# Optimization experiments

Hardware: AMD Instinct MI355X
Metric: run time of the kernel (lower is better)

The kernel has to match this reference:

```python
import jax, jax.numpy as jnp
import numpy as np

MU = 255          # mu-law levels - 1
H = 64            # block_hidden_size
SKIP = 256        # skip_size
NL = 24           # num_layers
CYC = 6           # cycle_size -> dilation = 2**(i % CYC)
UPK = 4           # upsample conv kernel/stride
REP = 75          # upsample repeat
LF = 80           # local_features_size
B = 2
LLEN = 64                      # local (spectrogram) frames
SLEN = LLEN * UPK * REP        # 19200 signal samples


def setup_inputs() -> dict:
    key = jax.random.key(0)
    ks = jax.random.split(key, 16)
    s = 0.1
    rn = lambda k, shape: jax.random.normal(k, shape, jnp.float32) * s
    return {
        "local_features": jax.random.normal(ks[0], (B, LLEN, LF), jnp.float32),
        "gold_signal": jax.random.randint(ks[1], (B, SLEN), 0, MU + 1, jnp.int32),
        "embed_W": rn(ks[2], (H, MU + 1)),          # 1x1 conv (mu+1 -> H), as matrix
        "embed_b": rn(ks[3], (H,)),
        "up_W": rn(ks[4], (LF, LF, UPK)),           # ConvTranspose1d weight [in, out, k]
        "up_b": rn(ks[5], (LF,)),
        "cond_W": rn(ks[6], (NL * 2 * H, LF)),      # 1x1 conv LF -> NL*2H
        "cond_b": rn(ks[7], (NL * 2 * H,)),
        "dil_W": rn(ks[8], (NL, 2 * H, H, 2)),      # dilated causal conv, kernel 2
        "dil_b": rn(ks[9], (NL, 2 * H)),
        "skip_W": rn(ks[10], (NL, SKIP, H)),
        "skip_b": rn(ks[11], (NL, SKIP)),
        "res_W": rn(ks[12], (NL - 1, H, H)),        # no residual conv on last layer
        "res_b": rn(ks[13], (NL - 1, H)),
        "out_W1": rn(ks[14], (MU + 1, SKIP)),       # out conv 1 (no bias)
        "out_W2": rn(ks[15], (MU + 1, MU + 1)),     # out conv 2 (no bias)
    }


def reference(local_features, gold_signal, embed_W, embed_b, up_W, up_b,
              cond_W, cond_b, dil_W, dil_b, skip_W, skip_b, res_W, res_b,
              out_W1, out_W2):
    Bv = local_features.shape[0]
    # --- conditional features upsample ---
    x = jnp.transpose(local_features, (0, 2, 1))                     # [B, LF, Lloc]
    # ConvTranspose1d with kernel == stride == UPK: each frame emits UPK frames
    up = jnp.einsum('bct,cok->botk', x, up_W).reshape(Bv, LF, -1)    # [B, LF, Lloc*UPK]
    up = up + up_b[None, :, None]
    up = jnp.repeat(up, REP, axis=-1)                                # [B, LF, SLEN]
    cond = jnp.einsum('oc,bct->bot', cond_W, up) + cond_b[None, :, None]
    L = cond.shape[-1]
    cond = cond.reshape(Bv, NL, 2 * H, L)                            # per-layer 2H channels
    # --- embed mu-law one-hot signal (one-hot matmul == gather) ---
    sig = jnp.transpose(embed_W[:, gold_signal], (1, 0, 2)) + embed_b[None, :, None]  # [B, H, L]
    # --- residual blocks ---
    skip_sum = jnp.zeros((Bv, SKIP, L), cond.dtype)
    for i in range(NL):
        d = 2 ** (i % CYC)
        prev = jnp.pad(sig, ((0, 0), (0, 0), (d, 0)))[:, :, :L]      # causal shift by dilation
        a = (jnp.einsum('oc,bct->bot', dil_W[i, :, :, 0], prev)
             + jnp.einsum('oc,bct->bot', dil_W[i, :, :, 1], sig)
             + dil_b[i][None, :, None] + cond[:, i])
        z = jnp.tanh(a[:, :H]) * jax.nn.sigmoid(a[:, H:])            # gated activation
        skip_sum = skip_sum + jnp.einsum('oc,bct->bot', skip_W[i], z) + skip_b[i][None, :, None]
        if i < NL - 1:
            sig = sig + jnp.einsum('oc,bct->bot', res_W[i], z) + res_b[i][None, :, None]
    # --- output head: ReLU -> 1x1 -> ReLU -> 1x1 -> log_softmax over levels ---
    h = jax.nn.relu(skip_sum)
    h = jax.nn.relu(jnp.einsum('oc,bct->bot', out_W1, h))
    logits = jnp.einsum('oc,bct->bot', out_W2, h)
    return jax.nn.log_softmax(logits, axis=1)                        # [B, mu+1, SLEN]
```

## Files before the change

kernel.cpp:

```cpp
#include <hip/hip_runtime.h>
#include <math.h>

#define MU1   256
#define H     64
#define H2    128
#define SKIPC 256
#define NL    24
#define LF    80
#define UPK   4
#define REP   75
#define BB    2
#define LLEN  64
#define LL    19200

using bf16x8 = __attribute__((ext_vector_type(8))) short;
using bf16x4 = __attribute__((ext_vector_type(4))) short;
using f32x4  = __attribute__((ext_vector_type(4))) float;

__device__ __forceinline__ float b2f(short s) {
    union { unsigned u; float f; } v; v.u = ((unsigned)(unsigned short)s) << 16; return v.f;
}
__device__ __forceinline__ short f2b(float f) {
    union { float f; unsigned u; } v; v.f = f;
    unsigned r = (v.u + 0x7fff + ((v.u >> 16) & 1)) >> 16;
    return (short)r;
}

__global__ __launch_bounds__(256) void prep_kernel(
    const float* __restrict__ dil_W,  const float* __restrict__ skip_W,
    const float* __restrict__ res_W,  const float* __restrict__ embed_W,
    const float* __restrict__ embed_b,const float* __restrict__ cond_W,
    const float* __restrict__ out_W1, const float* __restrict__ out_W2,
    const float* __restrict__ skip_b,
    short* __restrict__ dil_Wb, short* __restrict__ sWt,
    short* __restrict__ res_Wb, short* __restrict__ embed_allb,
    float* __restrict__ cond_Wt, short* __restrict__ W1b,
    short* __restrict__ W2b, float* __restrict__ sbsum)
{
    int idx = blockIdx.x * 256 + threadIdx.x;
    const int n1 = NL * 2 * H2 * H;
    const int n2 = 12 * 256 * 128;
    const int n3 = (NL - 1) * H * H;
    const int n4 = MU1 * H;
    const int n5 = LF * NL * H2;
    const int n6 = MU1 * SKIPC;
    const int n7 = MU1 * MU1;
    if (idx < n1) {
        int c = idx & 63; int o = (idx >> 6) & 127;
        int k = (idx >> 13) & 1; int i = idx >> 14;
        dil_Wb[idx] = f2b(dil_W[((i * H2 + o) * H + c) * 2 + k]);
        return;
    }
    idx -= n1;
    if (idx < n2) {
        int kc = idx & 127; int s = (idx >> 7) & 255; int ck = idx >> 15;
        sWt[idx] = f2b(skip_W[((2 * ck + (kc >> 6)) * SKIPC + s) * H + (kc & 63)]);
        return;
    }
    idx -= n2;
    if (idx < n3) { res_Wb[idx] = f2b(res_W[idx]); return; }
    idx -= n3;
    if (idx < n4) {
        int h = idx & 63; int g = idx >> 6;
        embed_allb[idx] = f2b(embed_W[h * MU1 + g] + embed_b[h]);
        return;
    }
    idx -= n4;
    if (idx < n5) {
        int o = idx % (NL * H2); int c = idx / (NL * H2);
        cond_Wt[idx] = cond_W[o * LF + c];
        return;
    }
    idx -= n5;
    if (idx < n6) { W1b[idx] = f2b(out_W1[idx]); return; }
    idx -= n6;
    if (idx < n7) { W2b[idx] = f2b(out_W2[idx]); return; }
    idx -= n7;
    if (idx < SKIPC) {
        float a = 0.f;
        for (int i = 0; i < NL; i++) a += skip_b[i * SKIPC + idx];
        sbsum[idx] = a;
        return;
    }
}

__global__ __launch_bounds__(256) void embed_kernel(
    const int* __restrict__ gold, const short* __restrict__ eW,
    short* __restrict__ sig)
{
    int idx = blockIdx.x * 256 + threadIdx.x;
    if (idx >= BB * LL * 8) return;
    int ch = idx & 7; int bt = idx >> 3;
    int g = gold[bt];
    *(bf16x8*)(sig + (size_t)bt * H + ch * 8) = *(const bf16x8*)(eW + g * H + ch * 8);
}

__global__ __launch_bounds__(256) void cond_kernel(
    const float* __restrict__ lf, const float* __restrict__ up_W,
    const float* __restrict__ up_b, const float* __restrict__ cond_Wt,
    const float* __restrict__ cond_b, const float* __restrict__ dil_b,
    float* __restrict__ condS)
{
    __shared__ float s_up[LF];
    int j = blockIdx.x;
    int ot = blockIdx.y;
    int b = blockIdx.z;
    int frame = j >> 2, k = j & 3;
    int tid = threadIdx.x;
    if (tid < LF) {
        float a = up_b[tid];
        const float* lfr = lf + (b * LLEN + frame) * LF;
        #pragma unroll 8
        for (int c = 0; c < LF; ++c) a += lfr[c] * up_W[(c * LF + tid) * UPK + k];
        s_up[tid] = a;
    }
    __syncthreads();
    int o = ot * 256 + tid;
    float a = cond_b[o] + dil_b[o];
    #pragma unroll 8
    for (int c = 0; c < LF; ++c) a += cond_Wt[c * 3072 + o] * s_up[c];
    condS[((size_t)(b * 256 + j)) * 3072 + o] = a;
}

template<int DA, int DB, bool LASTPAIR>
__global__ __launch_bounds__(256) void pair_mfma(
    const short* __restrict__ sig_in, short* __restrict__ sig_out,
    short* __restrict__ z12,
    const short* __restrict__ dil_Wb_all,
    const short* __restrict__ res_Wb_all,
    const float* __restrict__ res_b_all,
    const float* __restrict__ condS,
    int p, int slot)
{
    __shared__ __align__(16) short sa[144][72];
    __shared__ __align__(16) short sb[128][72];
    __shared__ __align__(16) short sz[128][72];
    __shared__ float scond[2][3][128];

    const int iA = 2 * p, iB = 2 * p + 1;
    const int b = blockIdx.y;
    const int t0 = blockIdx.x * 96;
    const int tid = threadIdx.x;
    const int w = tid >> 6;
    const int lane = tid & 63;
    const int lr = lane & 15, lg = lane >> 4;
    const int c0 = (t0 >= 32) ? (t0 - 32) / 75 : 0;

    {
        const short* basein = sig_in + (size_t)b * LL * H;
        #pragma unroll
        for (int it = 0; it < 5; ++it) {
            int task = tid + it * 256;
            if (task < 1152) {
                int r = task >> 3, ch = task & 7;
                int t = t0 - 48 + r;
                bf16x8 v = {};
                if (t >= 0) v = *(const bf16x8*)(basein + (size_t)t * H + ch * 8);
                *(bf16x8*)&sa[r][ch * 8] = v;
            }
        }
        #pragma unroll
        for (int it = 0; it < 3; ++it) {
            int task = tid + it * 256;
            int sel = task >= 384;
            int cj = (task - sel * 384) >> 7;
            int o = task & 127;
            int col = c0 + cj; col = col > 255 ? 255 : col;
            scond[sel][cj][o] = condS[((size_t)(b * 256 + col)) * 3072 + (iA + sel) * 128 + o];
        }
    }
    __syncthreads();

    {
        const short* dW = dil_Wb_all + (size_t)iA * 2 * H2 * H;
        f32x4 acc[2][8];
        #pragma unroll
        for (int m = 0; m < 2; ++m)
            #pragma unroll
            for (int n = 0; n < 8; ++n) acc[m][n] = (f32x4){0.f, 0.f, 0.f, 0.f};
        bf16x8 afA[2][4];
        #pragma unroll
        for (int m = 0; m < 2; ++m) {
            int rc = 16 + 16 * (2 * w + m) + lr;
            afA[m][0] = *(const bf16x8*)&sa[rc - DA][lg * 8];
            afA[m][1] = *(const bf16x8*)&sa[rc - DA][32 + lg * 8];
            afA[m][2] = *(const bf16x8*)&sa[rc][lg * 8];
            afA[m][3] = *(const bf16x8*)&sa[rc][32 + lg * 8];
        }
        #pragma unroll
        for (int n = 0; n < 8; ++n)
            #pragma unroll
            for (int kk = 0; kk < 4; ++kk) {
                bf16x8 bw = *(const bf16x8*)(dW + (((kk >> 1) * H2 + 16 * n + lr) * H) + (kk & 1) * 32 + lg * 8);
                acc[0][n] = __builtin_amdgcn_mfma_f32_16x16x32_bf16(afA[0][kk], bw, acc[0][n], 0, 0, 0);
                acc[1][n] = __builtin_amdgcn_mfma_f32_16x16x32_bf16(afA[1][kk], bw, acc[1][n], 0, 0, 0);
            }
        #pragma unroll
        for (int m = 0; m < 2; ++m)
            #pragma unroll
            for (int n = 0; n < 4; ++n)
                #pragma unroll
                for (int r = 0; r < 4; ++r) {
                    int relt = -32 + 16 * (2 * w + m) + 4 * lg + r;
                    int t = t0 + relt;
                    int o = 16 * n + lr;
                    short zb = 0;
                    if (t >= 0) {
                        int ci = t / 75 - c0;
                        float av = acc[m][n][r] + scond[0][ci][o];
                        float gv = acc[m][n + 4][r] + scond[0][ci][64 + o];
                        float th = 1.f - 2.f / (__expf(2.f * av) + 1.f);
                        float sg = 1.f / (1.f + __expf(-gv));
                        zb = f2b(th * sg);
                    }
                    sz[relt + 32][o] = zb;
                }
    }
    __syncthreads();

    #pragma unroll
    for (int it = 0; it < 3; ++it) {
        int task = tid + it * 256;
        int r = task >> 3, ch = task & 7;
        *(bf16x8*)(z12 + ((size_t)((slot * BB + b) * LL) + t0 + r) * 128 + ch * 8)
            = *(const bf16x8*)&sz[32 + r][ch * 8];
    }

    {
        const short* rW = res_Wb_all + (size_t)iA * H * H;
        const float* rb_ = res_b_all + (size_t)iA * H;
        f32x4 rac[2][4];
        #pragma unroll
        for (int m = 0; m < 2; ++m)
            #pragma unroll
            for (int n = 0; n < 4; ++n) rac[m][n] = (f32x4){0.f, 0.f, 0.f, 0.f};
        bf16x8 za[2][2];
        #pragma unroll
        for (int m = 0; m < 2; ++m) {
            int row = 16 * (2 * w + m) + lr;
            za[m][0] = *(const bf16x8*)&sz[row][lg * 8];
            za[m][1] = *(const bf16x8*)&sz[row][32 + lg * 8];
        }
        #pragma unroll
        for (int n = 0; n < 4; ++n)
            #pragma unroll
            for (int kk = 0; kk < 2; ++kk) {
                bf16x8 bw = *(const bf16x8*)(rW + (16 * n + lr) * H + kk * 32 + lg * 8);
                rac[0][n] = __builtin_amdgcn_mfma_f32_16x16x32_bf16(za[0][kk], bw, rac[0][n], 0, 0, 0);
                rac[1][n] = __builtin_amdgcn_mfma_f32_16x16x32_bf16(za[1][kk], bw, rac[1][n], 0, 0, 0);
            }
        #pragma unroll
        for (int n = 0; n < 4; ++n) {
            float rbv = rb_[16 * n + lr];
            #pragma unroll
            for (int m = 0; m < 2; ++m)
                #pragma unroll
                for (int r = 0; r < 4; ++r) {
                    int relt = -32 + 16 * (2 * w + m) + 4 * lg + r;
                    int t = t0 + relt;
                    int c = 16 * n + lr;
                    short vb = 0;
                    if (t >= 0) vb = f2b(b2f(sa[relt + 48][c]) + rac[m][n][r] + rbv);
                    sb[relt + 32][c] = vb;
                }
        }
    }
    __syncthreads();

    {
        const short* dW = dil_Wb_all + (size_t)iB * 2 * H2 * H;
        f32x4 accF[6], accG[6];
        #pragma unroll
        for (int m = 0; m < 6; ++m) { accF[m] = (f32x4){0.f,0.f,0.f,0.f}; accG[m] = (f32x4){0.f,0.f,0.f,0.f}; }
        bf16x8 bwF[4], bwG[4];
        #pragma unroll
        for (int kk = 0; kk < 4; ++kk) {
            int oF = 16 * w + lr;
            bwF[kk] = *(const bf16x8*)(dW + (((kk >> 1) * H2 + oF) * H) + (kk & 1) * 32 + lg * 8);
            bwG[kk] = *(const bf16x8*)(dW + (((kk >> 1) * H2 + 64 + oF) * H) + (kk & 1) * 32 + lg * 8);
        }
        #pragma unroll
        for (int m = 0; m < 6; ++m) {
            int rc = 32 + 16 * m + lr;
            bf16x8 af[4];
            af[0] = *(const bf16x8*)&sb[rc - DB][lg * 8];
            af[1] = *(const bf16x8*)&sb[rc - DB][32 + lg * 8];
            af[2] = *(const bf16x8*)&sb[rc][lg * 8];
            af[3] = *(const bf16x8*)&sb[rc][32 + lg * 8];
            #pragma unroll
            for (int kk = 0; kk < 4; ++kk)
                accF[m] = __builtin_amdgcn_mfma_f32_16x16x32_bf16(af[kk], bwF[kk], accF[m], 0, 0, 0);
            #pragma unroll
            for (int kk = 0; kk < 4; ++kk)
                accG[m] = __builtin_amdgcn_mfma_f32_16x16x32_bf16(af[kk], bwG[kk], accG[m], 0, 0, 0);
        }
        #pragma unroll
        for (int m = 0; m < 6; ++m)
            #pragma unroll
            for (int r = 0; r < 4; ++r) {
                int relt = 16 * m + 4 * lg + r;
                int t = t0 + relt;
                int o = 16 * w + lr;
                int ci = t / 75 - c0;
                float av = accF[m][r] + scond[1][ci][o];
                float gv = accG[m][r] + scond[1][ci][64 + o];
                float th = 1.f - 2.f / (__expf(2.f * av) + 1.f);
                float sg = 1.f / (1.f + __expf(-gv));
                sz[relt][o] = f2b(th * sg);
            }
    }
    __syncthreads();

    #pragma unroll
    for (int it = 0; it < 3; ++it) {
        int task = tid + it * 256;
        int r = task >> 3, ch = task & 7;
        *(bf16x8*)(z12 + ((size_t)((slot * BB + b) * LL) + t0 + r) * 128 + 64 + ch * 8)
            = *(const bf16x8*)&sz[r][ch * 8];
    }

    if (!LASTPAIR) {
        const short* rW = res_Wb_all + (size_t)iB * H * H;
        const float* rb_ = res_b_all + (size_t)iB * H;
        int c = 16 * w + lr;
        f32x4 rac[6];
        #pragma unroll
        for (int m = 0; m < 6; ++m) rac[m] = (f32x4){0.f, 0.f, 0.f, 0.f};
        bf16x8 bwR[2];
        bwR[0] = *(const bf16x8*)(rW + c * H + lg * 8);
        bwR[1] = *(const bf16x8*)(rW + c * H + 32 + lg * 8);
        #pragma unroll
        for (int m = 0; m < 6; ++m) {
            bf16x8 z0 = *(const bf16x8*)&sz[16 * m + lr][lg * 8];
            bf16x8 z1 = *(const bf16x8*)&sz[16 * m + lr][32 + lg * 8];
            rac[m] = __builtin_amdgcn_mfma_f32_16x16x32_bf16(z0, bwR[0], rac[m], 0, 0, 0);
            rac[m] = __builtin_amdgcn_mfma_f32_16x16x32_bf16(z1, bwR[1], rac[m], 0, 0, 0);
        }
        float rbv = rb_[c];
        #pragma unroll
        for (int m = 0; m < 6; ++m)
            #pragma unroll
            for (int r = 0; r < 4; ++r) {
                int relt = 16 * m + 4 * lg + r;
                sa[relt][c] = f2b(b2f(sb[relt + 32][c]) + rac[m][r] + rbv);
            }
        __syncthreads();
        #pragma unroll
        for (int it = 0; it < 3; ++it) {
            int task = tid + it * 256;
            int r = task >> 3, ch = task & 7;
            *(bf16x8*)(sig_out + ((size_t)(b * LL + t0 + r)) * H + ch * 8)
                = *(const bf16x8*)&sa[r][ch * 8];
        }
    }
}

__global__ __launch_bounds__(256) void skip12_kernel(
    const short* __restrict__ z12, const short* __restrict__ sWt,
    short* __restrict__ skipP)
{
    __shared__ __align__(16) short s_a[2][64][136];
    const int b = blockIdx.y;
    const int t0 = blockIdx.x * 64;
    const int tid = threadIdx.x;
    const int w = tid >> 6;
    const int lane = tid & 63;
    const int lr = lane & 15, lg = lane >> 4;

    f32x4 acc[4][4];
    #pragma unroll
    for (int mt = 0; mt < 4; ++mt)
        #pragma unroll
        for (int nt = 0; nt < 4; ++nt) acc[mt][nt] = (f32x4){0.f, 0.f, 0.f, 0.f};

    #pragma unroll
    for (int it = 0; it < 4; ++it) {
        int task = tid + it * 256;
        int r = task >> 4, ch = task & 15;
        *(bf16x8*)&s_a[0][r][ch * 8] =
            *(const bf16x8*)(z12 + ((size_t)(b * LL) + t0 + r) * 128 + ch * 8);
    }
    __syncthreads();

    for (int ck = 0; ck < 6; ++ck) {
        if (ck < 5) {
            #pragma unroll
            for (int it = 0; it < 4; ++it) {
                int task = tid + it * 256;
                int r = task >> 4, ch = task & 15;
                *(bf16x8*)&s_a[(ck + 1) & 1][r][ch * 8] =
                    *(const bf16x8*)(z12 + ((size_t)(((ck + 1) * BB + b) * LL) + t0 + r) * 128 + ch * 8);
            }
        }
        const short* wbase = sWt + ((size_t)ck << 15);
        const short (*buf)[136] = s_a[ck & 1];
        #pragma unroll
        for (int kk = 0; kk < 4; ++kk) {
            bf16x8 afr[4];
            #pragma unroll
            for (int mt = 0; mt < 4; ++mt)
                afr[mt] = *(const bf16x8*)&buf[16 * mt + lr][32 * kk + 8 * lg];
            #pragma unroll
            for (int nt = 0; nt < 4; ++nt) {
                bf16x8 bw = *(const bf16x8*)(wbase + ((64 * w + 16 * nt + lr) << 7) + 32 * kk + 8 * lg);
                #pragma unroll
                for (int mt = 0; mt < 4; ++mt)
                    acc[mt][nt] = __builtin_amdgcn_mfma_f32_16x16x32_bf16(afr[mt], bw, acc[mt][nt], 0, 0, 0);
            }
        }
        __syncthreads();
    }

    #pragma unroll
    for (int mt = 0; mt < 4; ++mt)
        #pragma unroll
        for (int nt = 0; nt < 4; ++nt) {
            int s = 64 * w + 16 * nt + lr;
            #pragma unroll
            for (int reg = 0; reg < 4; ++reg) {
                int t = t0 + 16 * mt + 4 * lg + reg;
                skipP[((size_t)(b * LL) + t) * 256 + s] = f2b(acc[mt][nt][reg]);
            }
        }
}

__global__ __launch_bounds__(256) void skiphead_kernel(
    const short* __restrict__ z12, const short* __restrict__ sWt,
    const short* __restrict__ skipP, const float* __restrict__ sbsum,
    const short* __restrict__ W1b, const short* __restrict__ W2b,
    float* __restrict__ out)
{
    __shared__ __align__(16) unsigned char smem[36864];
    short (*s_ab)[64][136] = (short(*)[64][136])smem;
    short (*s_x)[264] = (short(*)[264])smem;
    float (*s_o)[68]  = (float(*)[68])smem;
    __shared__ float s_red[4][64];
    __shared__ float s_sb[256];

    const int b = blockIdx.y;
    const int t0 = blockIdx.x * 64;
    const int tid = threadIdx.x;
    const int w = tid >> 6;
    const int lane = tid & 63;
    const int lr = lane & 15, lg = lane >> 4;

    s_sb[tid] = sbsum[tid];

    f32x4 acc[4][4];
    #pragma unroll
    for (int mt = 0; mt < 4; ++mt)
        #pragma unroll
        for (int nt = 0; nt < 4; ++nt) acc[mt][nt] = (f32x4){0.f, 0.f, 0.f, 0.f};

    #pragma unroll
    for (int it = 0; it < 4; ++it) {
        int task = tid + it * 256;
        int r = task >> 4, ch = task & 15;
        *(bf16x8*)&s_ab[0][r][ch * 8] =
            *(const bf16x8*)(z12 + ((size_t)(b * LL) + t0 + r) * 128 + ch * 8);
    }
    __syncthreads();
    for (int ck = 0; ck < 6; ++ck) {
        if (ck < 5) {
            #pragma unroll
            for (int it = 0; it < 4; ++it) {
                int task = tid + it * 256;
                int r = task >> 4, ch = task & 15;
                *(bf16x8*)&s_ab[(ck + 1) & 1][r][ch * 8] =
                    *(const bf16x8*)(z12 + ((size_t)(((ck + 1) * BB + b) * LL) + t0 + r) * 128 + ch * 8);
            }
        }
        const short* wbase = sWt + ((size_t)(6 + ck) << 15);
        const short (*buf)[136] = s_ab[ck & 1];
        #pragma unroll
        for (int kk = 0; kk < 4; ++kk) {
            bf16x8 afr[4];
            #pragma unroll
            for (int mt = 0; mt < 4; ++mt)
                afr[mt] = *(const bf16x8*)&buf[16 * mt + lr][32 * kk + 8 * lg];
            #pragma unroll
            for (int nt = 0; nt < 4; ++nt) {
                bf16x8 bw = *(const bf16x8*)(wbase + ((64 * w + 16 * nt + lr) << 7) + 32 * kk + 8 * lg);
                #pragma unroll
                for (int mt = 0; mt < 4; ++mt)
                    acc[mt][nt] = __builtin_amdgcn_mfma_f32_16x16x32_bf16(afr[mt], bw, acc[mt][nt], 0, 0, 0);
            }
        }
        __syncthreads();
    }

    #pragma unroll
    for (int it = 0; it < 8; ++it) {
        int task = tid + it * 256;
        int r = task >> 5, ch = task & 31;
        *(bf16x8*)&s_x[r][ch * 8] =
            *(const bf16x8*)(skipP + ((size_t)(b * LL) + t0 + r) * 256 + ch * 8);
    }
    __syncthreads();
    #pragma unroll
    for (int mt = 0; mt < 4; ++mt)
        #pragma unroll
        for (int nt = 0; nt < 4; ++nt) {
            int s = 64 * w + 16 * nt + lr;
            #pragma unroll
            for (int reg = 0; reg < 4; ++reg) {
                int tl = 16 * mt + 4 * lg + reg;
                float v = acc[mt][nt][reg] + b2f(s_x[tl][s]) + s_sb[s];
                s_x[tl][s] = f2b(fmaxf(v, 0.f));
            }
        }
    __syncthreads();

    f32x4 acc1[4][4];
    #pragma unroll
    for (int mt = 0; mt < 4; ++mt)
        #pragma unroll
        for (int nt = 0; nt < 4; ++nt) acc1[mt][nt] = (f32x4){0.f, 0.f, 0.f, 0.f};
    #pragma unroll
    for (int kk = 0; kk < 8; ++kk) {
        bf16x8 afr[4];
        #pragma unroll
        for (int mt = 0; mt < 4; ++mt)
            afr[mt] = *(const bf16x8*)&s_x[16 * mt + lr][32 * kk + 8 * lg];
        #pragma unroll
        for (int nt = 0; nt < 4; ++nt) {
            bf16x8 bw = *(const bf16x8*)(W1b + ((size_t)(64 * w + 16 * nt + lr)) * MU1 + 32 * kk + 8 * lg);
            #pragma unroll
            for (int mt = 0; mt < 4; ++mt)
                acc1[mt][nt] = __builtin_amdgcn_mfma_f32_16x16x32_bf16(afr[mt], bw, acc1[mt][nt], 0, 0, 0);
        }
    }
    __syncthreads();
    #pragma unroll
    for (int mt = 0; mt < 4; ++mt)
        #pragma unroll
        for (int nt = 0; nt < 4; ++nt)
            #pragma unroll
            for (int reg = 0; reg < 4; ++reg) {
                int tl = 16 * mt + 4 * lg + reg;
                int o = 64 * w + 16 * nt + lr;
                s_x[tl][o] = f2b(fmaxf(acc1[mt][nt][reg], 0.f));
            }
    __syncthreads();

    f32x4 acc2[4][4];
    #pragma unroll
    for (int mt = 0; mt < 4; ++mt)
        #pragma unroll
        for (int nt = 0; nt < 4; ++nt) acc2[mt][nt] = (f32x4){0.f, 0.f, 0.f, 0.f};
    #pragma unroll
    for (int kk = 0; kk < 8; ++kk) {
        bf16x8 afr[4];
        #pragma unroll
        for (int mt = 0; mt < 4; ++mt)
            afr[mt] = *(const bf16x8*)&s_x[16 * mt + lr][32 * kk + 8 * lg];
        #pragma unroll
        for (int nt = 0; nt < 4; ++nt) {
            bf16x8 bw = *(const bf16x8*)(W2b + ((size_t)(64 * w + 16 * nt + lr)) * MU1 + 32 * kk + 8 * lg);
            #pragma unroll
            for (int mt = 0; mt < 4; ++mt)
                acc2[mt][nt] = __builtin_amdgcn_mfma_f32_16x16x32_bf16(afr[mt], bw, acc2[mt][nt], 0, 0, 0);
        }
    }

    float mv[4][4];
    #pragma unroll
    for (int mt = 0; mt < 4; ++mt)
        #pragma unroll
        for (int reg = 0; reg < 4; ++reg) {
            float m = -3.4e38f;
            #pragma unroll
            for (int nt = 0; nt < 4; ++nt) m = fmaxf(m, acc2[mt][nt][reg]);
            #pragma unroll
            for (int off = 1; off <= 8; off <<= 1) m = fmaxf(m, __shfl_xor(m, off));
            int tl = 16 * mt + 4 * lg + reg;
            if (lr == 0) s_red[w][tl] = m;
        }
    __syncthreads();
    #pragma unroll
    for (int mt = 0; mt < 4; ++mt)
        #pragma unroll
        for (int reg = 0; reg < 4; ++reg) {
            int tl = 16 * mt + 4 * lg + reg;
            mv[mt][reg] = fmaxf(fmaxf(s_red[0][tl], s_red[1][tl]), fmaxf(s_red[2][tl], s_red[3][tl]));
        }
    __syncthreads();
    #pragma unroll
    for (int mt = 0; mt < 4; ++mt)
        #pragma unroll
        for (int reg = 0; reg < 4; ++reg) {
            float s = 0.f;
            #pragma unroll
            for (int nt = 0; nt < 4; ++nt) s += __expf(acc2[mt][nt][reg] - mv[mt][reg]);
            #pragma unroll
            for (int off = 1; off <= 8; off <<= 1) s += __shfl_xor(s, off);
            int tl = 16 * mt + 4 * lg + reg;
            if (lr == 0) s_red[w][tl] = s;
        }
    __syncthreads();
    #pragma unroll
    for (int mt = 0; mt < 4; ++mt)
        #pragma unroll
        for (int reg = 0; reg < 4; ++reg) {
            int tl = 16 * mt + 4 * lg + reg;
            float denom = s_red[0][tl] + s_red[1][tl] + s_red[2][tl] + s_red[3][tl];
            mv[mt][reg] = mv[mt][reg] + __logf(denom);
        }
    __syncthreads();

    #pragma unroll
    for (int pass = 0; pass < 2; ++pass) {
        if ((w >> 1) == pass) {
            #pragma unroll
            for (int mt = 0; mt < 4; ++mt)
                #pragma unroll
                for (int nt = 0; nt < 4; ++nt)
                    #pragma unroll
                    for (int reg = 0; reg < 4; ++reg) {
                        int ch = 64 * (w & 1) + 16 * nt + lr;
                        int tl = 16 * mt + 4 * lg + reg;
                        s_o[ch][tl] = acc2[mt][nt][reg] - mv[mt][reg];
                    }
        }
        __syncthreads();
        {
            int row = tid >> 1, half = tid & 1;
            float* op = out + ((size_t)(b * MU1 + pass * 128 + row)) * LL + t0 + half * 32;
            #pragma unroll
            for (int k = 0; k < 8; ++k)
                *(f32x4*)(op + 4 * k) = *(const f32x4*)&s_o[row][half * 32 + 4 * k];
        }
        __syncthreads();
    }
}

extern "C" void kernel_launch(void* const* d_in, const int* in_sizes, int n_in,
                              void* d_out, int out_size, void* d_ws, size_t ws_size,
                              hipStream_t stream)
{
    const float* lf      = (const float*)d_in[0];
    const int*   gold    = (const int*)  d_in[1];
    const float* embed_W = (const float*)d_in[2];
    const float* embed_b = (const float*)d_in[3];
    const float* up_W    = (const float*)d_in[4];
    const float* up_b    = (const float*)d_in[5];
    const float* cond_W  = (const float*)d_in[6];
    const float* cond_b  = (const float*)d_in[7];
    const float* dil_W   = (const float*)d_in[8];
    const float* dil_b   = (const float*)d_in[9];
    const float* skip_W  = (const float*)d_in[10];
    const float* skip_b  = (const float*)d_in[11];
    const float* res_W   = (const float*)d_in[12];
    const float* res_b   = (const float*)d_in[13];
    const float* W1      = (const float*)d_in[14];
    const float* W2      = (const float*)d_in[15];
    float* out = (float*)d_out;

    unsigned char* p = (unsigned char*)d_ws;
    short* sigA      = (short*)p; p += (size_t)BB * LL * H * 2;
    short* sigB      = (short*)p; p += (size_t)BB * LL * H * 2;
    short* z12       = (short*)p; p += (size_t)6 * BB * LL * 128 * 2;
    short* skipP     = (short*)p; p += (size_t)BB * LL * SKIPC * 2;
    float* condS     = (float*)p; p += (size_t)BB * 256 * NL * H2 * 4;
    short* dil_Wb    = (short*)p; p += (size_t)NL * 2 * H2 * H * 2;
    short* sWt       = (short*)p; p += (size_t)12 * 256 * 128 * 2;
    short* res_Wb    = (short*)p; p += (size_t)(NL - 1) * H * H * 2;
    short* embed_allb= (short*)p; p += (size_t)MU1 * H * 2;
    float* cond_Wt   = (float*)p; p += (size_t)LF * NL * H2 * 4;
    short* W1b       = (short*)p; p += (size_t)MU1 * SKIPC * 2;
    short* W2b       = (short*)p; p += (size_t)MU1 * MU1 * 2;
    float* sbsum     = (float*)p; p += (size_t)SKIPC * 4;

    const int prep_n = NL*2*H2*H + 12*256*128 + (NL-1)*H*H + MU1*H + LF*NL*H2 + MU1*SKIPC + MU1*MU1 + SKIPC;
    prep_kernel<<<(prep_n + 255) / 256, 256, 0, stream>>>(
        dil_W, skip_W, res_W, embed_W, embed_b, cond_W, W1, W2, skip_b,
        dil_Wb, sWt, res_Wb, embed_allb, cond_Wt, W1b, W2b, sbsum);

    embed_kernel<<<(BB * LL * 8 + 255) / 256, 256, 0, stream>>>(gold, embed_allb, sigA);

    cond_kernel<<<dim3(256, 12, BB), 256, 0, stream>>>(lf, up_W, up_b, cond_Wt, cond_b, dil_b, condS);

    short* si = sigA;
    short* so = sigB;
    dim3 pgrid(LL / 96, BB);
    dim3 sgrid(LL / 64, BB);
    for (int pp = 0; pp < 12; ++pp) {
        int slot = pp % 6;
        int r3 = pp % 3;
        if (r3 == 0)
            pair_mfma<1, 2, false><<<pgrid, 256, 0, stream>>>(si, so, z12, dil_Wb, res_Wb, res_b, condS, pp, slot);
        else if (r3 == 1)
            pair_mfma<4, 8, false><<<pgrid, 256, 0, stream>>>(si, so, z12, dil_Wb, res_Wb, res_b, condS, pp, slot);
        else if (pp == 11)
            pair_mfma<16, 32, true><<<pgrid, 256, 0, stream>>>(si, so, z12, dil_Wb, res_Wb, res_b, condS, pp, slot);
        else
            pair_mfma<16, 32, false><<<pgrid, 256, 0, stream>>>(si, so, z12, dil_Wb, res_Wb, res_b, condS, pp, slot);
        short* tmp = si; si = so; so = tmp;

        if (pp == 5)
            skip12_kernel<<<sgrid, 256, 0, stream>>>(z12, sWt, skipP);
    }

    skiphead_kernel<<<sgrid, 256, 0, stream>>>(z12, sWt, skipP, sbsum, W1b, W2b, out);
}
```

Measured before the change: 559.0 us.

## Restructure skip and head kernels as single-wave blocks over 32-step tiles

The skip-accumulation and output-head kernels now run as one-wavefront blocks, each covering 32 time steps and all 256 output channels. A-fragments are read straight from global memory instead of being staged in double-buffered shared memory. Because one wave owns every channel of a row, log-softmax reduces with shuffles only, with no cross-wave shared reductions or block barriers. The cost is a large per-lane accumulator footprint (32 f32x4 tiles), which risks register pressure and low occupancy, and weight fragments are now reloaded by twice as many blocks.

```diff
diff --git a/kernel.cpp b/kernel.cpp
--- a/kernel.cpp
+++ b/kernel.cpp
@@ -355,282 +355,192 @@
     }
 }
 
-__global__ __launch_bounds__(256) void skip12_kernel(
+__global__ __launch_bounds__(64, 2) void skipk_wave(
     const short* __restrict__ z12, const short* __restrict__ sWt,
     short* __restrict__ skipP)
 {
-    __shared__ __align__(16) short s_a[2][64][136];
+    __shared__ __align__(16) short s_x[32][264];
     const int b = blockIdx.y;
-    const int t0 = blockIdx.x * 64;
-    const int tid = threadIdx.x;
-    const int w = tid >> 6;
-    const int lane = tid & 63;
+    const int t0 = blockIdx.x * 32;
+    const int lane = threadIdx.x;
     const int lr = lane & 15, lg = lane >> 4;
 
-    f32x4 acc[4][4];
-    #pragma unroll
-    for (int mt = 0; mt < 4; ++mt)
-        #pragma unroll
-        for (int nt = 0; nt < 4; ++nt) acc[mt][nt] = (f32x4){0.f, 0.f, 0.f, 0.f};
-
-    #pragma unroll
-    for (int it = 0; it < 4; ++it) {
-        int task = tid + it * 256;
-        int r = task >> 4, ch = task & 15;
-        *(bf16x8*)&s_a[0][r][ch * 8] =
-            *(const bf16x8*)(z12 + ((size_t)(b * LL) + t0 + r) * 128 + ch * 8);
-    }
-    __syncthreads();
+    f32x4 acc[2][16];
+    #pragma unroll
+    for (int mt = 0; mt < 2; ++mt)
+        #pragma unroll
+        for (int nt = 0; nt < 16; ++nt) acc[mt][nt] = (f32x4){0.f, 0.f, 0.f, 0.f};
 
     for (int ck = 0; ck < 6; ++ck) {
-        if (ck < 5) {
-            #pragma unroll
-            for (int it = 0; it < 4; ++it) {
-                int task = tid + it * 256;
-                int r = task >> 4, ch = task & 15;
-                *(bf16x8*)&s_a[(ck + 1) & 1][r][ch * 8] =
-                    *(const bf16x8*)(z12 + ((size_t)(((ck + 1) * BB + b) * LL) + t0 + r) * 128 + ch * 8);
-            }
-        }
-        const short* wbase = sWt + ((size_t)ck << 15);
-        const short (*buf)[136] = s_a[ck & 1];
+        const short* zb = z12 + ((size_t)((ck * BB + b) * LL) + t0) * 128;
+        const short* wb = sWt + ((size_t)ck << 15);
         #pragma unroll
         for (int kk = 0; kk < 4; ++kk) {
-            bf16x8 afr[4];
-            #pragma unroll
-            for (int mt = 0; mt < 4; ++mt)
-                afr[mt] = *(const bf16x8*)&buf[16 * mt + lr][32 * kk + 8 * lg];
-            #pragma unroll
-            for (int nt = 0; nt < 4; ++nt) {
-                bf16x8 bw = *(const bf16x8*)(wbase + ((64 * w + 16 * nt + lr) << 7) + 32 * kk + 8 * lg);
-                #pragma unroll
-                for (int mt = 0; mt < 4; ++mt)
-                    acc[mt][nt] = __builtin_amdgcn_mfma_f32_16x16x32_bf16(afr[mt], bw, acc[mt][nt], 0, 0, 0);
-            }
-        }
-        __syncthreads();
-    }
-
-    #pragma unroll
-    for (int mt = 0; mt < 4; ++mt)
-        #pragma unroll
-        for (int nt = 0; nt < 4; ++nt) {
-            int s = 64 * w + 16 * nt + lr;
-            #pragma unroll
-            for (int reg = 0; reg < 4; ++reg) {
-                int t = t0 + 16 * mt + 4 * lg + reg;
-                skipP[((size_t)(b * LL) + t) * 256 + s] = f2b(acc[mt][nt][reg]);
-            }
-        }
-}
-
-__global__ __launch_bounds__(256) void skiphead_kernel(
+            bf16x8 af0 = *(const bf16x8*)(zb + lr * 128 + 32 * kk + 8 * lg);
+            bf16x8 af1 = *(const bf16x8*)(zb + (16 + lr) * 128 + 32 * kk + 8 * lg);
+            #pragma unroll
+            for (int nt = 0; nt < 16; ++nt) {
+                bf16x8 bw = *(const bf16x8*)(wb + ((16 * nt + lr) << 7) + 32 * kk + 8 * lg);
+                acc[0][nt] = __builtin_amdgcn_mfma_f32_16x16x32_bf16(af0, bw, acc[0][nt], 0, 0, 0);
+                acc[1][nt] = __builtin_amdgcn_mfma_f32_16x16x32_bf16(af1, bw, acc[1][nt], 0, 0, 0);
+            }
+        }
+    }
+    #pragma unroll
+    for (int mt = 0; mt < 2; ++mt)
+        #pragma unroll
+        for (int nt = 0; nt < 16; ++nt)
+            #pragma unroll
+            for (int reg = 0; reg < 4; ++reg)
+                s_x[16 * mt + 4 * lg + reg][16 * nt + lr] = f2b(acc[mt][nt][reg]);
+    #pragma unroll
+    for (int i = 0; i < 16; ++i) {
+        int idx = i * 64 + lane;
+        int r = idx >> 5, c8 = idx & 31;
+        *(bf16x8*)(skipP + ((size_t)(b * LL) + t0 + r) * 256 + c8 * 8)
+            = *(const bf16x8*)&s_x[r][c8 * 8];
+    }
+}
+
+__global__ __launch_bounds__(64, 2) void skiphead_wave(
     const short* __restrict__ z12, const short* __restrict__ sWt,
     const short* __restrict__ skipP, const float* __restrict__ sbsum,
     const short* __restrict__ W1b, const short* __restrict__ W2b,
     float* __restrict__ out)
 {
-    __shared__ __align__(16) unsigned char smem[36864];
-    short (*s_ab)[64][136] = (short(*)[64][136])smem;
+    __shared__ __align__(16) unsigned char smem[16896];
     short (*s_x)[264] = (short(*)[264])smem;
-    float (*s_o)[68]  = (float(*)[68])smem;
-    __shared__ float s_red[4][64];
-    __shared__ float s_sb[256];
+    float (*s_f)[33]  = (float(*)[33])smem;
 
     const int b = blockIdx.y;
-    const int t0 = blockIdx.x * 64;
-    const int tid = threadIdx.x;
-    const int w = tid >> 6;
-    const int lane = tid & 63;
+    const int t0 = blockIdx.x * 32;
+    const int lane = threadIdx.x;
     const int lr = lane & 15, lg = lane >> 4;
 
-    s_sb[tid] = sbsum[tid];
-
-    f32x4 acc[4][4];
-    #pragma unroll
-    for (int mt = 0; mt < 4; ++mt)
-        #pragma unroll
-        for (int nt = 0; nt < 4; ++nt) acc[mt][nt] = (f32x4){0.f, 0.f, 0.f, 0.f};
-
-    #pragma unroll
-    for (int it = 0; it < 4; ++it) {
-        int task = tid + it * 256;
-        int r = task >> 4, ch = task & 15;
-        *(bf16x8*)&s_ab[0][r][ch * 8] =
-            *(const bf16x8*)(z12 + ((size_t)(b * LL) + t0 + r) * 128 + ch * 8);
-    }
-    __syncthreads();
+    float sb[16];
+    #pragma unroll
+    for (int nt = 0; nt < 16; ++nt) sb[nt] = sbsum[16 * nt + lr];
+
+    f32x4 acc[2][16];
+    #pragma unroll
+    for (int mt = 0; mt < 2; ++mt)
+        #pragma unroll
+        for (int nt = 0; nt < 16; ++nt) acc[mt][nt] = (f32x4){0.f, 0.f, 0.f, 0.f};
+
     for (int ck = 0; ck < 6; ++ck) {
-        if (ck < 5) {
-            #pragma unroll
-            for (int it = 0; it < 4; ++it) {
-                int task = tid + it * 256;
-                int r = task >> 4, ch = task & 15;
-                *(bf16x8*)&s_ab[(ck + 1) & 1][r][ch * 8] =
-                    *(const bf16x8*)(z12 + ((size_t)(((ck + 1) * BB + b) * LL) + t0 + r) * 128 + ch * 8);
-            }
-        }
-        const short* wbase = sWt + ((size_t)(6 + ck) << 15);
-        const short (*buf)[136] = s_ab[ck & 1];
+        const short* zb = z12 + ((size_t)((ck * BB + b) * LL) + t0) * 128;
+        const short* wb = sWt + ((size_t)(6 + ck) << 15);
         #pragma unroll
         for (int kk = 0; kk < 4; ++kk) {
-            bf16x8 afr[4];
-            #pragma unroll
-            for (int mt = 0; mt < 4; ++mt)
-                afr[mt] = *(const bf16x8*)&buf[16 * mt + lr][32 * kk + 8 * lg];
-            #pragma unroll
-            for (int nt = 0; nt < 4; ++nt) {
-                bf16x8 bw = *(const bf16x8*)(wbase + ((64 * w + 16 * nt + lr) << 7) + 32 * kk + 8 * lg);
-                #pragma unroll
-                for (int mt = 0; mt < 4; ++mt)
-                    acc[mt][nt] = __builtin_amdgcn_mfma_f32_16x16x32_bf16(afr[mt], bw, acc[mt][nt], 0, 0, 0);
-            }
-        }
-        __syncthreads();
-    }
-
-    #pragma unroll
-    for (int it = 0; it < 8; ++it) {
-        int task = tid + it * 256;
-        int r = task >> 5, ch = task & 31;
-        *(bf16x8*)&s_x[r][ch * 8] =
-            *(const bf16x8*)(skipP + ((size_t)(b * LL) + t0 + r) * 256 + ch * 8);
-    }
-    __syncthreads();
-    #pragma unroll
-    for (int mt = 0; mt < 4; ++mt)
-        #pragma unroll
-        for (int nt = 0; nt < 4; ++nt) {
-            int s = 64 * w + 16 * nt + lr;
+            bf16x8 af0 = *(const bf16x8*)(zb + lr * 128 + 32 * kk + 8 * lg);
+            bf16x8 af1 = *(const bf16x8*)(zb + (16 + lr) * 128 + 32 * kk + 8 * lg);
+            #pragma unroll
+            for (int nt = 0; nt < 16; ++nt) {
+                bf16x8 bw = *(const bf16x8*)(wb + ((16 * nt + lr) << 7) + 32 * kk + 8 * lg);
+                acc[0][nt] = __builtin_amdgcn_mfma_f32_16x16x32_bf16(af0, bw, acc[0][nt], 0, 0, 0);
+                acc[1][nt] = __builtin_amdgcn_mfma_f32_16x16x32_bf16(af1, bw, acc[1][nt], 0, 0, 0);
+            }
+        }
+    }
+
+    #pragma unroll
+    for (int i = 0; i < 16; ++i) {
+        int idx = i * 64 + lane;
+        int r = idx >> 5, c8 = idx & 31;
+        *(bf16x8*)&s_x[r][c8 * 8]
+            = *(const bf16x8*)(skipP + ((size_t)(b * LL) + t0 + r) * 256 + c8 * 8);
+    }
+    #pragma unroll
+    for (int mt = 0; mt < 2; ++mt)
+        #pragma unroll
+        for (int nt = 0; nt < 16; ++nt)
             #pragma unroll
             for (int reg = 0; reg < 4; ++reg) {
-                int tl = 16 * mt + 4 * lg + reg;
-                float v = acc[mt][nt][reg] + b2f(s_x[tl][s]) + s_sb[s];
-                s_x[tl][s] = f2b(fmaxf(v, 0.f));
-            }
-        }
-    __syncthreads();
-
-    f32x4 acc1[4][4];
-    #pragma unroll
-    for (int mt = 0; mt < 4; ++mt)
-        #pragma unroll
-        for (int nt = 0; nt < 4; ++nt) acc1[mt][nt] = (f32x4){0.f, 0.f, 0.f, 0.f};
+                int tl = 16 * mt + 4 * lg + reg, ch = 16 * nt + lr;
+                float v = acc[mt][nt][reg] + b2f(s_x[tl][ch]) + sb[nt];
+                s_x[tl][ch] = f2b(fmaxf(v, 0.f));
+            }
+
+    f32x4 acc1[2][16];
+    #pragma unroll
+    for (int mt = 0; mt < 2; ++mt)
+        #pragma unroll
+        for (int nt = 0; nt < 16; ++nt) acc1[mt][nt] = (f32x4){0.f, 0.f, 0.f, 0.f};
     #pragma unroll
     for (int kk = 0; kk < 8; ++kk) {
-        bf16x8 afr[4];
-        #pragma unroll
-        for (int mt = 0; mt < 4; ++mt)
-            afr[mt] = *(const bf16x8*)&s_x[16 * mt + lr][32 * kk + 8 * lg];
-        #pragma unroll
-        for (int nt = 0; nt < 4; ++nt) {
-            bf16x8 bw = *(const bf16x8*)(W1b + ((size_t)(64 * w + 16 * nt + lr)) * MU1 + 32 * kk + 8 * lg);
-            #pragma unroll
-            for (int mt = 0; mt < 4; ++mt)
-                acc1[mt][nt] = __builtin_amdgcn_mfma_f32_16x16x32_bf16(afr[mt], bw, acc1[mt][nt], 0, 0, 0);
-        }
-    }
-    __syncthreads();
-    #pragma unroll
-    for (int mt = 0; mt < 4; ++mt)
-        #pragma unroll
-        for (int nt = 0; nt < 4; ++nt)
-            #pragma unroll
-            for (int reg = 0; reg < 4; ++reg) {
-                int tl = 16 * mt + 4 * lg + reg;
-                int o = 64 * w + 16 * nt + lr;
-                s_x[tl][o] = f2b(fmaxf(acc1[mt][nt][reg], 0.f));
-            }
-    __syncthreads();
-
-    f32x4 acc2[4][4];
-    #pragma unroll
-    for (int mt = 0; mt < 4; ++mt)
-        #pragma unroll
-        for (int nt = 0; nt < 4; ++nt) acc2[mt][nt] = (f32x4){0.f, 0.f, 0.f, 0.f};
+        bf16x8 af0 = *(const bf16x8*)&s_x[lr][32 * kk + 8 * lg];
+        bf16x8 af1 = *(const bf16x8*)&s_x[16 + lr][32 * kk + 8 * lg];
+        #pragma unroll
+        for (int nt = 0; nt < 16; ++nt) {
+            bf16x8 bw = *(const bf16x8*)(W1b + ((size_t)(16 * nt + lr)) * MU1 + 32 * kk + 8 * lg);
+            acc1[0][nt] = __builtin_amdgcn_mfma_f32_16x16x32_bf16(af0, bw, acc1[0][nt], 0, 0, 0);
+            acc1[1][nt] = __builtin_amdgcn_mfma_f32_16x16x32_bf16(af1, bw, acc1[1][nt], 0, 0, 0);
+        }
+    }
+    #pragma unroll
+    for (int mt = 0; mt < 2; ++mt)
+        #pragma unroll
+        for (int nt = 0; nt < 16; ++nt)
+            #pragma unroll
+            for (int reg = 0; reg < 4; ++reg)
+                s_x[16 * mt + 4 * lg + reg][16 * nt + lr] = f2b(fmaxf(acc1[mt][nt][reg], 0.f));
+
+    f32x4 acc2[2][16];
+    #pragma unroll
+    for (int mt = 0; mt < 2; ++mt)
+        #pragma unroll
+        for (int nt = 0; nt < 16; ++nt) acc2[mt][nt] = (f32x4){0.f, 0.f, 0.f, 0.f};
     #pragma unroll
     for (int kk = 0; kk < 8; ++kk) {
-        bf16x8 afr[4];
-        #pragma unroll
-        for (int mt = 0; mt < 4; ++mt)
-            afr[mt] = *(const bf16x8*)&s_x[16 * mt + lr][32 * kk + 8 * lg];
-        #pragma unroll
-        for (int nt = 0; nt < 4; ++nt) {
-            bf16x8 bw = *(const bf16x8*)(W2b + ((size_t)(64 * w + 16 * nt + lr)) * MU1 + 32 * kk + 8 * lg);
-            #pragma unroll
-            for (int mt = 0; mt < 4; ++mt)
-                acc2[mt][nt] = __builtin_amdgcn_mfma_f32_16x16x32_bf16(afr[mt], bw, acc2[mt][nt], 0, 0, 0);
-        }
-    }
-
-    float mv[4][4];
-    #pragma unroll
-    for (int mt = 0; mt < 4; ++mt)
+        bf16x8 af0 = *(const bf16x8*)&s_x[lr][32 * kk + 8 * lg];
+        bf16x8 af1 = *(const bf16x8*)&s_x[16 + lr][32 * kk + 8 * lg];
+        #pragma unroll
+        for (int nt = 0; nt < 16; ++nt) {
+            bf16x8 bw = *(const bf16x8*)(W2b + ((size_t)(16 * nt + lr)) * MU1 + 32 * kk + 8 * lg);
+            acc2[0][nt] = __builtin_amdgcn_mfma_f32_16x16x32_bf16(af0, bw, acc2[0][nt], 0, 0, 0);
+            acc2[1][nt] = __builtin_amdgcn_mfma_f32_16x16x32_bf16(af1, bw, acc2[1][nt], 0, 0, 0);
+        }
+    }
+
+    float lse[2][4];
+    #pragma unroll
+    for (int mt = 0; mt < 2; ++mt)
         #pragma unroll
         for (int reg = 0; reg < 4; ++reg) {
             float m = -3.4e38f;
             #pragma unroll
-            for (int nt = 0; nt < 4; ++nt) m = fmaxf(m, acc2[mt][nt][reg]);
+            for (int nt = 0; nt < 16; ++nt) m = fmaxf(m, acc2[mt][nt][reg]);
             #pragma unroll
             for (int off = 1; off <= 8; off <<= 1) m = fmaxf(m, __shfl_xor(m, off));
-            int tl = 16 * mt + 4 * lg + reg;
-            if (lr == 0) s_red[w][tl] = m;
-        }
-    __syncthreads();
-    #pragma unroll
-    for (int mt = 0; mt < 4; ++mt)
-        #pragma unroll
-        for (int reg = 0; reg < 4; ++reg) {
-            int tl = 16 * mt + 4 * lg + reg;
-            mv[mt][reg] = fmaxf(fmaxf(s_red[0][tl], s_red[1][tl]), fmaxf(s_red[2][tl], s_red[3][tl]));
-        }
-    __syncthreads();
-    #pragma unroll
-    for (int mt = 0; mt < 4; ++mt)
-        #pragma unroll
-        for (int reg = 0; reg < 4; ++reg) {
             float s = 0.f;
             #pragma unroll
-            for (int nt = 0; nt < 4; ++nt) s += __expf(acc2[mt][nt][reg] - mv[mt][reg]);
+            for (int nt = 0; nt < 16; ++nt) s += __expf(acc2[mt][nt][reg] - m);
             #pragma unroll
             for (int off = 1; off <= 8; off <<= 1) s += __shfl_xor(s, off);
-            int tl = 16 * mt + 4 * lg + reg;
-            if (lr == 0) s_red[w][tl] = s;
-        }
-    __syncthreads();
-    #pragma unroll
-    for (int mt = 0; mt < 4; ++mt)
-        #pragma unroll
-        for (int reg = 0; reg < 4; ++reg) {
-            int tl = 16 * mt + 4 * lg + reg;
-            float denom = s_red[0][tl] + s_red[1][tl] + s_red[2][tl] + s_red[3][tl];
-            mv[mt][reg] = mv[mt][reg] + __logf(denom);
-        }
-    __syncthreads();
+            lse[mt][reg] = m + __logf(s);
+        }
 
     #pragma unroll
     for (int pass = 0; pass < 2; ++pass) {
-        if ((w >> 1) == pass) {
-            #pragma unroll
-            for (int mt = 0; mt < 4; ++mt)
+        #pragma unroll
+        for (int mt = 0; mt < 2; ++mt)
+            #pragma unroll
+            for (int nt8 = 0; nt8 < 8; ++nt8)
                 #pragma unroll
-                for (int nt = 0; nt < 4; ++nt)
-                    #pragma unroll
-                    for (int reg = 0; reg < 4; ++reg) {
-                        int ch = 64 * (w & 1) + 16 * nt + lr;
-                        int tl = 16 * mt + 4 * lg + reg;
-                        s_o[ch][tl] = acc2[mt][nt][reg] - mv[mt][reg];
-                    }
-        }
-        __syncthreads();
-        {
-            int row = tid >> 1, half = tid & 1;
-            float* op = out + ((size_t)(b * MU1 + pass * 128 + row)) * LL + t0 + half * 32;
-            #pragma unroll
-            for (int k = 0; k < 8; ++k)
-                *(f32x4*)(op + 4 * k) = *(const f32x4*)&s_o[row][half * 32 + 4 * k];
-        }
-        __syncthreads();
+                for (int reg = 0; reg < 4; ++reg)
+                    s_f[16 * nt8 + lr][16 * mt + 4 * lg + reg]
+                        = acc2[mt][8 * pass + nt8][reg] - lse[mt][reg];
+        #pragma unroll
+        for (int i = 0; i < 16; ++i) {
+            int idx = i * 64 + lane;
+            int r = idx >> 3, c4 = idx & 7;
+            f32x4 v;
+            v[0] = s_f[r][c4 * 4 + 0];
+            v[1] = s_f[r][c4 * 4 + 1];
+            v[2] = s_f[r][c4 * 4 + 2];
+            v[3] = s_f[r][c4 * 4 + 3];
+            *(f32x4*)(out + ((size_t)(b * MU1 + 128 * pass + r)) * LL + t0 + c4 * 4) = v;
+        }
     }
 }
 
@@ -683,7 +593,7 @@
     short* si = sigA;
     short* so = sigB;
     dim3 pgrid(LL / 96, BB);
-    dim3 sgrid(LL / 64, BB);
+    dim3 wgrid(LL / 32, BB);
     for (int pp = 0; pp < 12; ++pp) {
         int slot = pp % 6;
         int r3 = pp % 3;
@@ -698,8 +608,8 @@
         short* tmp = si; si = so; so = tmp;
 
         if (pp == 5)
-            skip12_kernel<<<sgrid, 256, 0, stream>>>(z12, sWt, skipP);
-    }
-
-    skiphead_kernel<<<sgrid, 256, 0, stream>>>(z12, sWt, skipP, sbsum, W1b, W2b, out);
-}
+            skipk_wave<<<wgrid, 64, 0, stream>>>(z12, sWt, skipP);
+    }
+
+    skiphead_wave<<<wgrid, 64, 0, stream>>>(z12, sWt, skipP, sbsum, W1b, W2b, out);
+}
```

Result: slower. 599.4 us (+7.2%).
